# Optimization experiments

Measured on AMD Instinct MI355X. Metric: run time of the kernel, lower is better.

## Reference

```python
import jax, jax.numpy as jnp
import numpy as np
from jax.scipy.linalg import expm

# dims: batch B_, seq S_, d_inner Di, d_state Ds (must equal Di), dt_rank R
B_, S_, Di, Ds, R = 16, 512, 64, 64, 4


def setup_inputs() -> dict:
    key = jax.random.key(0)
    k0, k1, k2, k3 = jax.random.split(key, 4)
    x = jax.random.normal(k0, (B_, S_, Di), dtype=jnp.float32)
    # x_proj: Linear(Di -> R + 2*Ds); small init keeps dt small so expm stays finite
    Wx = jax.random.normal(k1, (R + 2 * Ds, Di), dtype=jnp.float32) * 0.05
    bx = jax.random.normal(k2, (R + 2 * Ds,), dtype=jnp.float32) * 0.05
    # dt_proj: Linear(R -> Di)
    Wdt = jax.random.normal(k3, (Di, R), dtype=jnp.float32) * 0.01
    bdt = jnp.zeros((Di,), dtype=jnp.float32)
    # A_log[d, n] = log(n+1), matching repeat(arange(1..Ds), 'n -> d n')
    A_log = jnp.log(jnp.broadcast_to(jnp.arange(1, Ds + 1, dtype=jnp.float32), (Di, Ds)))
    Dp = jnp.ones((Di,), dtype=jnp.float32)
    return {"x": x, "Wx": Wx, "bx": bx, "Wdt": Wdt, "bdt": bdt, "A_log": A_log, "Dp": Dp}


def _ssm_forward(x, Wx, bx, Wdt, bdt, A_log, Dp):
    b = x.shape[0]
    A = -jnp.exp(A_log)                    # (Di, Ds)
    I = jnp.eye(Di, Ds, dtype=x.dtype)     # (Di, Ds), square here
    expm_b = jax.vmap(expm)                # batched matrix exponential

    def step(hs, xi):
        # xi: (b, Di)
        proj = xi @ Wx.T + bx              # (b, R + 2*Ds)
        Bm = proj[:, :Ds]                  # (b, Ds)
        dtr = proj[:, Ds:Ds + R]           # (b, R)
        Cm = proj[:, Ds + R:]              # (b, Ds)
        dt = dtr @ Wdt.T + bdt             # (b, Di)
        deltaA = dt[:, :, None] * A[None]  # (b, Di, Ds) = diag(dt) @ A
        dA = expm_b(deltaA)                # exact discretization: exp(dt*A)
        deltaB = dt[:, :, None] * Bm[:, None, :]           # (b, Di, Ds)
        dB = jnp.linalg.pinv(deltaA) @ (dA - I) @ deltaB   # (dtA)^+ (e^{dtA}-I) dtB
        hs = hs * dA + xi[:, :, None] * dB
        mask = (jnp.abs(xi).sum(-1) > 1e-5).astype(x.dtype)[:, None, None]
        hs = hs * mask + jax.lax.stop_gradient(hs) * (1.0 - mask)
        hs = jnp.clip(hs, -1e6, 1e6)
        y = jnp.einsum('bdn,bn->bd', hs, Cm) + Dp * xi
        return hs, (y, hs)

    hs0 = jnp.zeros((b, Di, Ds), dtype=x.dtype)
    _, (ys, hss) = jax.lax.scan(step, hs0, jnp.swapaxes(x, 0, 1))
    # original returns (y of the LAST timestep, all hidden states (b, seq, Di, Ds))
    return ys[-1], jnp.swapaxes(hss, 0, 1)


def reference(x, Wx, bx, Wdt, bdt, A_log, Dp):
    return _ssm_forward(x, Wx, bx, Wdt, bdt, A_log, Dp)
```

## Files before the change

kernel.cpp:

```cpp
#include <hip/hip_runtime.h>
#include <cmath>

#define B_  16
#define S_  512
#define DI  64
#define DS  64
#define RR  4
#define CH  8
#define CL  64
#define CLIPM 1.0e6f

#define WS_U    524288
#define WS_BM   1048576
#define WS_CML  1572864
#define WS_HIN  1573888

#define SUMN 524288

__device__ __forceinline__ float clampM(float v) {
    return fminf(fmaxf(v, -CLIPM), CLIPM);
}

__global__ __launch_bounds__(64)
void ssm_k1(const float* __restrict__ x, const float* __restrict__ Wx,
            const float* __restrict__ bx, const float* __restrict__ Wdt,
            const float* __restrict__ bdt, const float* __restrict__ A_log,
            float* __restrict__ ws)
{
    __shared__ float xs[DI];
    __shared__ float aa_s[DS];
    __shared__ float dtr_s[RR];
    const int bt   = blockIdx.x;
    const int lane = threadIdx.x;

    const float xv = x[bt * DI + lane];
    xs[lane]   = xv;
    aa_s[lane] = -expf(A_log[lane]);
    __syncthreads();

    float accB = bx[lane];
    {
        const float* wr = Wx + lane * DI;
        #pragma unroll
        for (int i = 0; i < DI; i += 4) {
            float4 w = *reinterpret_cast<const float4*>(wr + i);
            accB += w.x * xs[i] + w.y * xs[i + 1] + w.z * xs[i + 2] + w.w * xs[i + 3];
        }
    }
    if (lane < RR) {
        float acc = bx[DS + lane];
        const float* wr = Wx + (DS + lane) * DI;
        #pragma unroll
        for (int i = 0; i < DI; i += 4) {
            float4 w = *reinterpret_cast<const float4*>(wr + i);
            acc += w.x * xs[i] + w.y * xs[i + 1] + w.z * xs[i + 2] + w.w * xs[i + 3];
        }
        dtr_s[lane] = acc;
    }
    __syncthreads();

    float dtv = bdt[lane];
    #pragma unroll
    for (int r = 0; r < RR; ++r) dtv += dtr_s[r] * Wdt[lane * RR + r];

    const float a_l = aa_s[lane];

    float sv = a_l * dtv;
    float qv = a_l * a_l;
    #pragma unroll
    for (int off = 32; off > 0; off >>= 1) {
        sv += __shfl_xor(sv, off);
        qv += __shfl_xor(qv, off);
    }

    const float E   = expm1f(sv);
    const float phi = (fabsf(sv) < 1e-3f)
                        ? fmaf(sv, fmaf(sv, 1.0f / 6.0f, 0.5f), 1.0f)
                        : (E / sv);

    ws[bt * DI + lane]          = phi * dtv;
    ws[WS_U + bt * DI + lane]   = xv * (E / qv) * a_l;
    ws[WS_BM + bt * DI + lane]  = accB;

    if ((bt & (S_ - 1)) == (S_ - 1)) {
        float accC = bx[DS + RR + lane];
        const float* wr = Wx + (DS + RR + lane) * DI;
        #pragma unroll
        for (int i = 0; i < DI; i += 4) {
            float4 w = *reinterpret_cast<const float4*>(wr + i);
            accC += w.x * xs[i] + w.y * xs[i + 1] + w.z * xs[i + 2] + w.w * xs[i + 3];
        }
        ws[WS_CML + (bt >> 9) * DS + lane] = accC;
    }
}

__global__ __launch_bounds__(256)
void ssm_k2a(const float* __restrict__ ws, const float* __restrict__ A_log,
             float* __restrict__ out)
{
    const int tid  = threadIdx.x;
    const int n    = tid & 63;
    const int d    = ((blockIdx.x >> 3) & 15) * 4 + (tid >> 6);
    const int c    = blockIdx.x & 7;
    const int b    = blockIdx.x >> 7;

    const float a_n   = -expf(A_log[n]);
    const float delta = (d == n) ? 1.0f : 0.0f;

    const float* phidt = ws + (size_t)(b * S_) * DI + d;
    const float* uws   = ws + WS_U + (size_t)(b * S_) * DI + d;
    const float* bmws  = ws + WS_BM + (size_t)(b * S_) * DI + n;

    const int t0 = c * CL;
    float alpha = 1.0f, beta = 0.0f, lo = -CLIPM, hi = CLIPM;
    #pragma unroll 8
    for (int j = 0; j < CL; ++j) {
        const int t = t0 + j;
        const float pv = phidt[(size_t)t * DI];
        const float uv = uws[(size_t)t * DI];
        const float bv = bmws[(size_t)t * DI];
        const float av = fmaf(pv, a_n, delta);
        const float w  = uv * bv;
        alpha = av * alpha;
        beta  = fmaf(av, beta, w);
        const float t1 = fmaf(av, lo, w);
        const float t2 = fmaf(av, hi, w);
        lo = clampM(fminf(t1, t2));
        hi = clampM(fmaxf(t1, t2));
    }
    const size_t si = (((size_t)b * CH + c) * DI + d) * DS + n;
    float* sum = out + 1024;
    sum[si]            = alpha;
    sum[SUMN + si]     = beta;
    sum[2 * SUMN + si] = lo;
    sum[3 * SUMN + si] = hi;
}

__global__ __launch_bounds__(256)
void ssm_k2b(float* __restrict__ ws, const float* __restrict__ out)
{
    const int tid = threadIdx.x;
    const int n   = tid & 63;
    const int d   = (blockIdx.x & 15) * 4 + (tid >> 6);
    const int b   = blockIdx.x >> 4;

    const float* sum = out + 1024;
    float* hin = ws + WS_HIN;

    float h = 0.0f;
    #pragma unroll
    for (int c = 0; c < CH; ++c) {
        const size_t si = (((size_t)b * CH + c) * DI + d) * DS + n;
        hin[si] = h;
        const float alpha = sum[si];
        const float beta  = sum[SUMN + si];
        const float lo    = sum[2 * SUMN + si];
        const float hi    = sum[3 * SUMN + si];
        h = fminf(fmaxf(fmaf(alpha, h, beta), lo), hi);
    }
}

__global__ __launch_bounds__(256)
void ssm_k2c(const float* __restrict__ ws, const float* __restrict__ x,
             const float* __restrict__ A_log, const float* __restrict__ Dp,
             float* __restrict__ out)
{
    const int tid = threadIdx.x;
    const int n   = tid & 63;
    const int d   = ((blockIdx.x >> 3) & 15) * 4 + (tid >> 6);
    const int c   = blockIdx.x & 7;
    const int b   = blockIdx.x >> 7;

    const float a_n   = -expf(A_log[n]);
    const float delta = (d == n) ? 1.0f : 0.0f;

    const float* phidt = ws + (size_t)(b * S_) * DI + d;
    const float* uws   = ws + WS_U + (size_t)(b * S_) * DI + d;
    const float* bmws  = ws + WS_BM + (size_t)(b * S_) * DI + n;

    const size_t si = (((size_t)b * CH + c) * DI + d) * DS + n;
    float h = ws[WS_HIN + si];

    float* po = out + 1024 + (size_t)(b * S_) * (DI * DS) + d * DS + n;
    const int t0 = c * CL;
    #pragma unroll 8
    for (int j = 0; j < CL; ++j) {
        const int t = t0 + j;
        const float pv = phidt[(size_t)t * DI];
        const float uv = uws[(size_t)t * DI];
        const float bv = bmws[(size_t)t * DI];
        const float av = fmaf(pv, a_n, delta);
        h = fmaf(av, h, uv * bv);
        h = clampM(h);
        po[(size_t)t * (DI * DS)] = h;
    }

    if (c == CH - 1) {
        float v = h * ws[WS_CML + b * DS + n];
        #pragma unroll
        for (int off = 32; off > 0; off >>= 1) v += __shfl_xor(v, off);
        if (n == 0) {
            const float xi = x[((b * S_) + S_ - 1) * DI + d];
            out[b * DI + d] = v + Dp[d] * xi;
        }
    }
}

extern "C" void kernel_launch(void* const* d_in, const int* in_sizes, int n_in,
                              void* d_out, int out_size, void* d_ws, size_t ws_size,
                              hipStream_t stream)
{
    const float* x     = (const float*)d_in[0];
    const float* Wx    = (const float*)d_in[1];
    const float* bx    = (const float*)d_in[2];
    const float* Wdt   = (const float*)d_in[3];
    const float* bdt   = (const float*)d_in[4];
    const float* A_log = (const float*)d_in[5];
    const float* Dp    = (const float*)d_in[6];
    float* out = (float*)d_out;
    float* ws  = (float*)d_ws;

    ssm_k1 <<<B_ * S_, 64, 0, stream>>>(x, Wx, bx, Wdt, bdt, A_log, ws);
    ssm_k2a<<<B_ * 16 * CH, 256, 0, stream>>>(ws, A_log, out);
    ssm_k2b<<<B_ * 16, 256, 0, stream>>>(ws, out);
    ssm_k2c<<<B_ * 16 * CH, 256, 0, stream>>>(ws, x, A_log, Dp, out);
}
```

Baseline: 70.70 us.

## Give each thread four state columns with vector loads and interleaved chunk summaries

The three scan kernels now give each thread four consecutive state columns (n) instead of one. The B values and the chunk summaries are read and written as float4, and the summary layout is changed to interleaved alpha/beta/lo/hi records. The hidden-state output uses 16-byte nontemporal stores, and the final y reduction shrinks to a 16-lane shuffle. This cuts per-element address math and load instructions and widens the memory transactions. In exchange it launches four times fewer blocks, which lowers parallelism for the sequential scans, and raises register use per thread.

```diff
diff --git a/kernel.cpp b/kernel.cpp
--- a/kernel.cpp
+++ b/kernel.cpp
@@ -10,12 +10,13 @@
 #define CL  64
 #define CLIPM 1.0e6f
 
+typedef float f32x4 __attribute__((ext_vector_type(4)));
+
 #define WS_U    524288
 #define WS_BM   1048576
 #define WS_CML  1572864
 #define WS_HIN  1573888
 
-#define SUMN 524288
 
 __device__ __forceinline__ float clampM(float v) {
     return fminf(fmaxf(v, -CLIPM), CLIPM);
@@ -28,14 +29,13 @@
             float* __restrict__ ws)
 {
     __shared__ float xs[DI];
-    __shared__ float aa_s[DS];
     __shared__ float dtr_s[RR];
     const int bt   = blockIdx.x;
     const int lane = threadIdx.x;
 
     const float xv = x[bt * DI + lane];
-    xs[lane]   = xv;
-    aa_s[lane] = -expf(A_log[lane]);
+    xs[lane] = xv;
+    const float a_l = -expf(A_log[lane]);
     __syncthreads();
 
     float accB = bx[lane];
@@ -43,7 +43,7 @@
         const float* wr = Wx + lane * DI;
         #pragma unroll
         for (int i = 0; i < DI; i += 4) {
-            float4 w = *reinterpret_cast<const float4*>(wr + i);
+            f32x4 w = *reinterpret_cast<const f32x4*>(wr + i);
             accB += w.x * xs[i] + w.y * xs[i + 1] + w.z * xs[i + 2] + w.w * xs[i + 3];
         }
     }
@@ -52,7 +52,7 @@
         const float* wr = Wx + (DS + lane) * DI;
         #pragma unroll
         for (int i = 0; i < DI; i += 4) {
-            float4 w = *reinterpret_cast<const float4*>(wr + i);
+            f32x4 w = *reinterpret_cast<const f32x4*>(wr + i);
             acc += w.x * xs[i] + w.y * xs[i + 1] + w.z * xs[i + 2] + w.w * xs[i + 3];
         }
         dtr_s[lane] = acc;
@@ -62,8 +62,6 @@
     float dtv = bdt[lane];
     #pragma unroll
     for (int r = 0; r < RR; ++r) dtv += dtr_s[r] * Wdt[lane * RR + r];
-
-    const float a_l = aa_s[lane];
 
     float sv = a_l * dtv;
     float qv = a_l * a_l;
@@ -87,119 +85,149 @@
         const float* wr = Wx + (DS + RR + lane) * DI;
         #pragma unroll
         for (int i = 0; i < DI; i += 4) {
-            float4 w = *reinterpret_cast<const float4*>(wr + i);
+            f32x4 w = *reinterpret_cast<const f32x4*>(wr + i);
             accC += w.x * xs[i] + w.y * xs[i + 1] + w.z * xs[i + 2] + w.w * xs[i + 3];
         }
         ws[WS_CML + (bt >> 9) * DS + lane] = accC;
     }
 }
 
+
 __global__ __launch_bounds__(256)
-void ssm_k2a(const float* __restrict__ ws, const float* __restrict__ A_log,
-             float* __restrict__ out)
-{
-    const int tid  = threadIdx.x;
-    const int n    = tid & 63;
-    const int d    = ((blockIdx.x >> 3) & 15) * 4 + (tid >> 6);
-    const int c    = blockIdx.x & 7;
-    const int b    = blockIdx.x >> 7;
-
-    const float a_n   = -expf(A_log[n]);
-    const float delta = (d == n) ? 1.0f : 0.0f;
+void ssm_kA(const float* __restrict__ ws, const float* __restrict__ A_log,
+            float* __restrict__ out)
+{
+    const int tid = threadIdx.x;
+    const int c   = blockIdx.x & 7;
+    const int dg  = (blockIdx.x >> 3) & 3;
+    const int b   = blockIdx.x >> 5;
+    const int dl  = tid >> 4;
+    const int n0  = (tid & 15) << 2;
+    const int d   = dg * 16 + dl;
+
+    const f32x4 alog4 = *reinterpret_cast<const f32x4*>(A_log + n0);
+    float an[4]  = { -expf(alog4.x), -expf(alog4.y), -expf(alog4.z), -expf(alog4.w) };
+    float dlt[4];
+    #pragma unroll
+    for (int k = 0; k < 4; ++k) dlt[k] = (d == n0 + k) ? 1.0f : 0.0f;
 
     const float* phidt = ws + (size_t)(b * S_) * DI + d;
-    const float* uws   = ws + WS_U + (size_t)(b * S_) * DI + d;
-    const float* bmws  = ws + WS_BM + (size_t)(b * S_) * DI + n;
-
-    const int t0 = c * CL;
-    float alpha = 1.0f, beta = 0.0f, lo = -CLIPM, hi = CLIPM;
-    #pragma unroll 8
-    for (int j = 0; j < CL; ++j) {
-        const int t = t0 + j;
-        const float pv = phidt[(size_t)t * DI];
-        const float uv = uws[(size_t)t * DI];
-        const float bv = bmws[(size_t)t * DI];
-        const float av = fmaf(pv, a_n, delta);
-        const float w  = uv * bv;
-        alpha = av * alpha;
-        beta  = fmaf(av, beta, w);
-        const float t1 = fmaf(av, lo, w);
-        const float t2 = fmaf(av, hi, w);
-        lo = clampM(fminf(t1, t2));
-        hi = clampM(fmaxf(t1, t2));
-    }
-    const size_t si = (((size_t)b * CH + c) * DI + d) * DS + n;
-    float* sum = out + 1024;
-    sum[si]            = alpha;
-    sum[SUMN + si]     = beta;
-    sum[2 * SUMN + si] = lo;
-    sum[3 * SUMN + si] = hi;
-}
-
-__global__ __launch_bounds__(256)
-void ssm_k2b(float* __restrict__ ws, const float* __restrict__ out)
-{
-    const int tid = threadIdx.x;
-    const int n   = tid & 63;
-    const int d   = (blockIdx.x & 15) * 4 + (tid >> 6);
-    const int b   = blockIdx.x >> 4;
-
-    const float* sum = out + 1024;
-    float* hin = ws + WS_HIN;
-
-    float h = 0.0f;
-    #pragma unroll
-    for (int c = 0; c < CH; ++c) {
-        const size_t si = (((size_t)b * CH + c) * DI + d) * DS + n;
-        hin[si] = h;
-        const float alpha = sum[si];
-        const float beta  = sum[SUMN + si];
-        const float lo    = sum[2 * SUMN + si];
-        const float hi    = sum[3 * SUMN + si];
-        h = fminf(fmaxf(fmaf(alpha, h, beta), lo), hi);
-    }
-}
-
-__global__ __launch_bounds__(256)
-void ssm_k2c(const float* __restrict__ ws, const float* __restrict__ x,
-             const float* __restrict__ A_log, const float* __restrict__ Dp,
-             float* __restrict__ out)
-{
-    const int tid = threadIdx.x;
-    const int n   = tid & 63;
-    const int d   = ((blockIdx.x >> 3) & 15) * 4 + (tid >> 6);
-    const int c   = blockIdx.x & 7;
-    const int b   = blockIdx.x >> 7;
-
-    const float a_n   = -expf(A_log[n]);
-    const float delta = (d == n) ? 1.0f : 0.0f;
-
-    const float* phidt = ws + (size_t)(b * S_) * DI + d;
-    const float* uws   = ws + WS_U + (size_t)(b * S_) * DI + d;
-    const float* bmws  = ws + WS_BM + (size_t)(b * S_) * DI + n;
-
-    const size_t si = (((size_t)b * CH + c) * DI + d) * DS + n;
-    float h = ws[WS_HIN + si];
-
-    float* po = out + 1024 + (size_t)(b * S_) * (DI * DS) + d * DS + n;
+    const float* uws   = ws + WS_U  + (size_t)(b * S_) * DI + d;
+    const float* bmp   = ws + WS_BM + (size_t)(b * S_) * DI + n0;
+
+    float al[4], be[4], lo[4], hi[4];
+    #pragma unroll
+    for (int k = 0; k < 4; ++k) { al[k] = 1.0f; be[k] = 0.0f; lo[k] = -CLIPM; hi[k] = CLIPM; }
+
     const int t0 = c * CL;
     #pragma unroll 8
     for (int j = 0; j < CL; ++j) {
         const int t = t0 + j;
         const float pv = phidt[(size_t)t * DI];
         const float uv = uws[(size_t)t * DI];
-        const float bv = bmws[(size_t)t * DI];
-        const float av = fmaf(pv, a_n, delta);
-        h = fmaf(av, h, uv * bv);
-        h = clampM(h);
-        po[(size_t)t * (DI * DS)] = h;
+        const f32x4 bv = *reinterpret_cast<const f32x4*>(bmp + (size_t)t * DI);
+        const float bva[4] = { bv.x, bv.y, bv.z, bv.w };
+        #pragma unroll
+        for (int k = 0; k < 4; ++k) {
+            const float av = fmaf(pv, an[k], dlt[k]);
+            const float w  = uv * bva[k];
+            al[k] = al[k] * av;
+            be[k] = fmaf(av, be[k], w);
+            const float u1 = fmaf(av, lo[k], w);
+            const float u2 = fmaf(av, hi[k], w);
+            lo[k] = clampM(fminf(u1, u2));
+            hi[k] = clampM(fmaxf(u1, u2));
+        }
+    }
+
+    f32x4* sum = reinterpret_cast<f32x4*>(out + 1024);
+    const size_t sb = (((size_t)b * CH + c) * DI + d) * DS + n0;
+    #pragma unroll
+    for (int k = 0; k < 4; ++k) {
+        f32x4 s = { al[k], be[k], lo[k], hi[k] };
+        sum[sb + k] = s;
+    }
+}
+
+__global__ __launch_bounds__(256)
+void ssm_kB(float* __restrict__ ws, const float* __restrict__ out)
+{
+    const int tid = threadIdx.x;
+    const int dg  = blockIdx.x & 3;
+    const int b   = blockIdx.x >> 2;
+    const int dl  = tid >> 4;
+    const int n0  = (tid & 15) << 2;
+    const int d   = dg * 16 + dl;
+
+    const f32x4* sum = reinterpret_cast<const f32x4*>(out + 1024);
+
+    float h[4] = { 0.0f, 0.0f, 0.0f, 0.0f };
+    #pragma unroll
+    for (int c = 0; c < CH; ++c) {
+        const size_t base = (((size_t)b * CH + c) * DI + d) * DS + n0;
+        f32x4 hv = { h[0], h[1], h[2], h[3] };
+        *reinterpret_cast<f32x4*>(ws + WS_HIN + base) = hv;
+        #pragma unroll
+        for (int k = 0; k < 4; ++k) {
+            const f32x4 s = sum[base + k];
+            h[k] = fminf(fmaxf(fmaf(s.x, h[k], s.y), s.z), s.w);
+        }
+    }
+}
+
+__global__ __launch_bounds__(256)
+void ssm_kC(const float* __restrict__ ws, const float* __restrict__ x,
+            const float* __restrict__ A_log, const float* __restrict__ Dp,
+            float* __restrict__ out)
+{
+    const int tid = threadIdx.x;
+    const int c   = blockIdx.x & 7;
+    const int dg  = (blockIdx.x >> 3) & 3;
+    const int b   = blockIdx.x >> 5;
+    const int dl  = tid >> 4;
+    const int n0  = (tid & 15) << 2;
+    const int d   = dg * 16 + dl;
+
+    const f32x4 alog4 = *reinterpret_cast<const f32x4*>(A_log + n0);
+    float an[4]  = { -expf(alog4.x), -expf(alog4.y), -expf(alog4.z), -expf(alog4.w) };
+    float dlt[4];
+    #pragma unroll
+    for (int k = 0; k < 4; ++k) dlt[k] = (d == n0 + k) ? 1.0f : 0.0f;
+
+    const size_t hbase = (((size_t)b * CH + c) * DI + d) * DS + n0;
+    const f32x4 h0 = *reinterpret_cast<const f32x4*>(ws + WS_HIN + hbase);
+    float h[4] = { h0.x, h0.y, h0.z, h0.w };
+
+    const float* phidt = ws + (size_t)(b * S_) * DI + d;
+    const float* uws   = ws + WS_U  + (size_t)(b * S_) * DI + d;
+    const float* bmp   = ws + WS_BM + (size_t)(b * S_) * DI + n0;
+
+    const int t0 = c * CL;
+    #pragma unroll 8
+    for (int j = 0; j < CL; ++j) {
+        const int t = t0 + j;
+        const float pv = phidt[(size_t)t * DI];
+        const float uv = uws[(size_t)t * DI];
+        const f32x4 bv = *reinterpret_cast<const f32x4*>(bmp + (size_t)t * DI);
+        const float bva[4] = { bv.x, bv.y, bv.z, bv.w };
+        #pragma unroll
+        for (int k = 0; k < 4; ++k) {
+            const float av = fmaf(pv, an[k], dlt[k]);
+            h[k] = clampM(fmaf(av, h[k], uv * bva[k]));
+        }
+        f32x4 hv = { h[0], h[1], h[2], h[3] };
+        float* po = out + 1024 + ((size_t)(b * S_ + t) * DI + d) * DS + n0;
+        __builtin_nontemporal_store(hv, reinterpret_cast<f32x4*>(po));
     }
 
     if (c == CH - 1) {
-        float v = h * ws[WS_CML + b * DS + n];
-        #pragma unroll
-        for (int off = 32; off > 0; off >>= 1) v += __shfl_xor(v, off);
-        if (n == 0) {
+        const f32x4 cm = *reinterpret_cast<const f32x4*>(ws + WS_CML + b * DS + n0);
+        float v = h[0] * cm.x + h[1] * cm.y + h[2] * cm.z + h[3] * cm.w;
+        v += __shfl_xor(v, 1);
+        v += __shfl_xor(v, 2);
+        v += __shfl_xor(v, 4);
+        v += __shfl_xor(v, 8);
+        if ((tid & 15) == 0) {
             const float xi = x[((b * S_) + S_ - 1) * DI + d];
             out[b * DI + d] = v + Dp[d] * xi;
         }
@@ -220,8 +248,8 @@
     float* out = (float*)d_out;
     float* ws  = (float*)d_ws;
 
-    ssm_k1 <<<B_ * S_, 64, 0, stream>>>(x, Wx, bx, Wdt, bdt, A_log, ws);
-    ssm_k2a<<<B_ * 16 * CH, 256, 0, stream>>>(ws, A_log, out);
-    ssm_k2b<<<B_ * 16, 256, 0, stream>>>(ws, out);
-    ssm_k2c<<<B_ * 16 * CH, 256, 0, stream>>>(ws, x, A_log, Dp, out);
-}
+    ssm_k1<<<B_ * S_, 64, 0, stream>>>(x, Wx, bx, Wdt, bdt, A_log, ws);
+    ssm_kA<<<B_ * 4 * CH, 256, 0, stream>>>(ws, A_log, out);
+    ssm_kB<<<B_ * 4, 256, 0, stream>>>(ws, out);
+    ssm_kC<<<B_ * 4 * CH, 256, 0, stream>>>(ws, x, A_log, Dp, out);
+}
```

Result: slower. 76.21 us (+7.8%).
